# Kernel tuning notes

Measured on AMD Instinct MI355X. Metric: run time of the kernel, lower is better.

## Reference

```python
import jax, jax.numpy as jnp
import numpy as np
from jax import lax

NUM_HEADS = 8


def setup_inputs() -> dict:
    key = jax.random.key(0)
    ks = jax.random.split(key, 6)
    B, L, Hd = 4, 4096, 512
    S = 45  # factor * ceil(ln(L)) = 5 * 9
    x = jax.random.normal(ks[0], (B, L, Hd), dtype=jnp.float32)
    scale = 1.0 / np.sqrt(Hd)
    Wq = jax.random.normal(ks[1], (Hd, Hd), dtype=jnp.float32) * scale
    Wk = jax.random.normal(ks[2], (Hd, Hd), dtype=jnp.float32) * scale
    Wv = jax.random.normal(ks[3], (Hd, Hd), dtype=jnp.float32) * scale
    Wo = jax.random.normal(ks[4], (Hd, Hd), dtype=jnp.float32) * scale
    index_sample = jax.random.randint(ks[5], (L, S), 0, L, dtype=jnp.int32)
    return {"x": x, "Wq": Wq, "Wk": Wk, "Wv": Wv, "Wo": Wo,
            "index_sample": index_sample}


def reference(x, Wq, Wk, Wv, Wo, index_sample):
    B, L, Hd = x.shape
    H = NUM_HEADS
    D = Hd // H
    S = index_sample.shape[1]
    u = S  # n_top active queries = factor*ceil(ln(L))

    def split_heads(t):  # [B,L,Hd] -> [B,H,L,D]
        return t.reshape(B, L, H, D).transpose(0, 2, 1, 3)

    q = split_heads(x @ Wq)
    k = split_heads(x @ Wk)
    v = split_heads(x @ Wv)

    scale = 1.0 / jnp.sqrt(jnp.asarray(D, dtype=x.dtype))

    # sampled key gather: [B,H,L,S,D]
    K_samp = k[:, :, index_sample, :]
    # sampled scores per query: [B,H,L,S]
    QK_samp = jnp.einsum('bhld,bhlsd->bhls', q, K_samp)
    # sparsity measurement: max - mean over sampled keys
    M = QK_samp.max(axis=-1) - QK_samp.mean(axis=-1)  # [B,H,L]
    _, top_idx = lax.top_k(M, u)                      # [B,H,u]

    # full attention only for active queries
    Qr = jnp.take_along_axis(q, top_idx[..., None], axis=2)   # [B,H,u,D]
    scores = jnp.einsum('bhud,bhld->bhul', Qr, k) * scale     # [B,H,u,L]
    attn = jax.nn.softmax(scores, axis=-1)
    ctx_sel = jnp.einsum('bhul,bhld->bhud', attn, v)          # [B,H,u,D]

    # inactive queries get mean(V); scatter active results in
    context = jnp.broadcast_to(v.mean(axis=2, keepdims=True), (B, H, L, D))
    b_idx = jnp.arange(B)[:, None, None]
    h_idx = jnp.arange(H)[None, :, None]
    context = context.at[b_idx, h_idx, top_idx].set(ctx_sel)

    out = context.transpose(0, 2, 1, 3).reshape(B, L, Hd) @ Wo
    return out
```

## Files before the change

kernel.cpp:

```cpp
#include <hip/hip_runtime.h>
#include <cmath>

#define SS 45
#define FSPLIT 16

typedef __attribute__((ext_vector_type(8))) _Float16 half8;
typedef __attribute__((ext_vector_type(4))) float float4v;
typedef __attribute__((ext_vector_type(8))) unsigned short ushort8v;

__device__ inline unsigned short f16b(float f) {
    union { _Float16 h; unsigned short u; } c;
    c.h = (_Float16)f;
    return c.u;
}
__device__ inline float f16back(unsigned short u) {
    union { _Float16 h; unsigned short u; } c;
    c.u = u;
    return (float)c.h;
}

__device__ __forceinline__ void async16(const void* g, void* l) {
    __builtin_amdgcn_global_load_lds(
        (const __attribute__((address_space(1))) void*)g,
        (__attribute__((address_space(3))) void*)l, 16, 0, 0);
}

template <int CTRL>
__device__ __forceinline__ float dppadd(float v) {
    int x = __builtin_amdgcn_mov_dpp(__float_as_int(v), CTRL, 0xF, 0xF, true);
    return v + __int_as_float(x);
}
template <int CTRL>
__device__ __forceinline__ float dppmax(float v) {
    int x = __builtin_amdgcn_mov_dpp(__float_as_int(v), CTRL, 0xF, 0xF, true);
    return fmaxf(v, __int_as_float(x));
}

__device__ __forceinline__ unsigned int fmono(float f) {
    unsigned int u = __float_as_uint(f);
    return (u & 0x80000000u) ? ~u : (u | 0x80000000u);
}

__global__ __launch_bounds__(256) void convW_kernel(
    const float* __restrict__ Wq, const float* __restrict__ Wk, const float* __restrict__ Wv,
    unsigned short* __restrict__ WTh, unsigned short* __restrict__ WTl,
    float* __restrict__ vmp)
{
    int bid = blockIdx.x;
    if (bid < 768) {
        int zy = bid >> 8;
        int bxy = bid & 255;
        const float* W = (zy == 0) ? Wq : (zy == 1) ? Wk : Wv;
        unsigned short* th = WTh + (size_t)zy * 262144;
        unsigned short* tl = WTl + (size_t)zy * 262144;
        __shared__ float t[32][33];
        int bx = bxy & 15, by = bxy >> 4;
        int tx = threadIdx.x & 31, ty = threadIdx.x >> 5;
        for (int i = ty; i < 32; i += 8) t[i][tx] = W[(size_t)(by * 32 + i) * 512 + bx * 32 + tx];
        __syncthreads();
        for (int i = ty; i < 32; i += 8) {
            float f = t[tx][i];
            unsigned short h = f16b(f);
            unsigned short lo = f16b(f - f16back(h));
            th[(size_t)(bx * 32 + i) * 512 + by * 32 + tx] = h;
            tl[(size_t)(bx * 32 + i) * 512 + by * 32 + tx] = lo;
        }
    } else {
        for (int i = threadIdx.x; i < 2048; i += 256) vmp[i] = 0.f;
    }
}

__global__ __launch_bounds__(512, 2) void qkv8_kernel(
    const float* __restrict__ X,
    const unsigned short* __restrict__ WTh, const unsigned short* __restrict__ WTl,
    float* __restrict__ Q, float* __restrict__ K, float* __restrict__ V,
    float* __restrict__ vmp)
{
    __shared__ unsigned short lds[73728];

    int wave = threadIdx.x >> 6;
    int lane = threadIdx.x & 63;
    int m0blk = blockIdx.x * 256;
    int n0blk = blockIdx.y * 128;
    int fr = lane & 15;
    int C = lane >> 4;
    int srow = lane >> 2;
    int sslot = lane & 3;
    int mrb = (wave >> 1) * 64;
    int nrb = (wave & 1) * 64;

    const unsigned short* gbB[5];
    gbB[0] = WTh;
    gbB[1] = WTl;
    gbB[2] = WTh + 262144;
    gbB[3] = WTl + 262144;
    gbB[4] = WTh + 524288;

    int rloc0 = wave * 32 + srow;
    int rloc1 = wave * 32 + 16 + srow;
    int Cp0 = sslot ^ ((rloc0 >> 1) & 3);
    int Cp1 = sslot ^ ((rloc1 >> 1) & 3);
    const float* xr0 = X + (size_t)(m0blk + rloc0) * 512 + Cp0 * 8;
    const float* xr1 = X + (size_t)(m0blk + rloc1) * 512 + Cp1 * 8;

    float4v accq[4][4], acck[4][4], accv[4][4];
    #pragma unroll
    for (int i = 0; i < 4; i++)
        #pragma unroll
        for (int j = 0; j < 4; j++) {
            accq[i][j] = (float4v){0.f, 0.f, 0.f, 0.f};
            acck[i][j] = (float4v){0.f, 0.f, 0.f, 0.f};
            accv[i][j] = (float4v){0.f, 0.f, 0.f, 0.f};
        }

    auto stageB = [&](int buf, int k0) {
        int rloc = wave * 16 + srow;
        int Cp = sslot ^ ((rloc >> 1) & 3);
        #pragma unroll
        for (int t = 0; t < 5; t++) {
            const unsigned short* g = gbB[t] + (size_t)(n0blk + rloc) * 512 + k0 + Cp * 8;
            async16(g, lds + buf * 36864 + 16384 + t * 4096 + wave * 512);
        }
    };

    float4 xv[2][2];
    auto loadX = [&](int k0) {
        xv[0][0] = *(const float4*)(xr0 + k0);
        xv[0][1] = *(const float4*)(xr0 + k0 + 4);
        xv[1][0] = *(const float4*)(xr1 + k0);
        xv[1][1] = *(const float4*)(xr1 + k0 + 4);
    };
    auto writeA = [&](int buf) {
        #pragma unroll
        for (int inst = 0; inst < 2; inst++) {
            const float* f = (const float*)&xv[inst][0];
            ushort8v hv, lv;
            #pragma unroll
            for (int e = 0; e < 8; e++) {
                unsigned short h = f16b(f[e]);
                hv[e] = h;
                lv[e] = f16b(f[e] - f16back(h));
            }
            unsigned short* dsth = lds + buf * 36864 + (wave * 32 + inst * 16) * 32 + lane * 8;
            *(ushort8v*)dsth = hv;
            *(ushort8v*)(dsth + 8192) = lv;
        }
    };

    loadX(0);
    stageB(0, 0);
    writeA(0);
    asm volatile("s_waitcnt vmcnt(0)" ::: "memory");
    asm volatile("s_waitcnt lgkmcnt(0)" ::: "memory");
    __builtin_amdgcn_s_barrier();

    for (int kk = 0; kk < 16; kk++) {
        const unsigned short* Lb = lds + (kk & 1) * 36864;
        int nbuf = (kk + 1) & 1;
        int nk0 = (kk + 1) * 32;

        if (kk < 15) {
            loadX(nk0);
            stageB(nbuf, nk0);
        }

        half8 A_h[4], A_l[4];
        #pragma unroll
        for (int i = 0; i < 4; i++) {
            int R = mrb + i * 16 + fr;
            int sl = C ^ ((R >> 1) & 3);
            A_h[i] = *(const half8*)(Lb + R * 32 + sl * 8);
            A_l[i] = *(const half8*)(Lb + 8192 + R * 32 + sl * 8);
        }
        #pragma unroll
        for (int j = 0; j < 4; j++) {
            int R = nrb + j * 16 + fr;
            int sl = C ^ ((R >> 1) & 3);
            int off = R * 32 + sl * 8;
            half8 Bqh = *(const half8*)(Lb + 16384 + off);
            half8 Bql = *(const half8*)(Lb + 20480 + off);
            half8 Bkh = *(const half8*)(Lb + 24576 + off);
            half8 Bkl = *(const half8*)(Lb + 28672 + off);
            half8 Bvh = *(const half8*)(Lb + 32768 + off);
            #pragma unroll
            for (int i = 0; i < 4; i++) {
                accq[i][j] = __builtin_amdgcn_mfma_f32_16x16x32_f16(A_h[i], Bqh, accq[i][j], 0, 0, 0);
                accq[i][j] = __builtin_amdgcn_mfma_f32_16x16x32_f16(A_h[i], Bql, accq[i][j], 0, 0, 0);
                accq[i][j] = __builtin_amdgcn_mfma_f32_16x16x32_f16(A_l[i], Bqh, accq[i][j], 0, 0, 0);
                acck[i][j] = __builtin_amdgcn_mfma_f32_16x16x32_f16(A_h[i], Bkh, acck[i][j], 0, 0, 0);
                acck[i][j] = __builtin_amdgcn_mfma_f32_16x16x32_f16(A_h[i], Bkl, acck[i][j], 0, 0, 0);
                acck[i][j] = __builtin_amdgcn_mfma_f32_16x16x32_f16(A_l[i], Bkh, acck[i][j], 0, 0, 0);
                accv[i][j] = __builtin_amdgcn_mfma_f32_16x16x32_f16(A_h[i], Bvh, accv[i][j], 0, 0, 0);
            }
        }

        if (kk < 15) {
            writeA(nbuf);
            asm volatile("s_waitcnt vmcnt(0)" ::: "memory");
            asm volatile("s_waitcnt lgkmcnt(0)" ::: "memory");
            __builtin_amdgcn_s_barrier();
        }
    }

    int hh = n0blk + nrb;
    int hd = hh >> 6;
    int bb0 = (m0blk + mrb) >> 12;
    {
        float cs[4];
        #pragma unroll
        for (int j = 0; j < 4; j++) {
            float s = 0.f;
            #pragma unroll
            for (int i = 0; i < 4; i++)
                #pragma unroll
                for (int r = 0; r < 4; r++) s += accv[i][j][r];
            s += __shfl_xor(s, 16, 64);
            s += __shfl_xor(s, 32, 64);
            cs[j] = s;
        }
        if (C == 0) {
            #pragma unroll
            for (int j = 0; j < 4; j++)
                atomicAdd(vmp + ((size_t)(bb0 * 8 + hd) * 64) + j * 16 + fr, cs[j]);
        }
    }

    int rbase = C * 4;
    int m0 = m0blk + mrb;
    #pragma unroll
    for (int i = 0; i < 4; i++)
        #pragma unroll
        for (int r = 0; r < 4; r++) {
            int rg = m0 + i * 16 + rbase + r;
            int bb = rg >> 12, l = rg & 4095;
            size_t rowoff = ((size_t)(bb * 8 + hd) * 4096 + l) * 64;
            #pragma unroll
            for (int j = 0; j < 4; j++) Q[rowoff + j * 16 + fr] = accq[i][j][r];
            #pragma unroll
            for (int j = 0; j < 4; j++) K[rowoff + j * 16 + fr] = acck[i][j][r];
            #pragma unroll
            for (int j = 0; j < 4; j++) V[rowoff + j * 16 + fr] = accv[i][j][r];
        }
}

__global__ __launch_bounds__(1024) void m_topk_kernel(
    const float* __restrict__ Q, const float* __restrict__ K,
    const int* __restrict__ idx, unsigned long long* __restrict__ cand)
{
    __shared__ unsigned long long keys[512];

    int bh = blockIdx.x & 31;
    int c = blockIdx.x >> 5;
    int wave = threadIdx.x >> 6;
    int lane = threadIdx.x & 63;
    int g = lane >> 3;
    int t = lane & 7;
    const float* kb = K + (size_t)bh * 4096 * 64;

    for (int ii = 0; ii < 32; ii++) {
        int l = c * 512 + wave * 32 + ii;
        int inst = bh * 4096 + l;
        float4 qa = *(const float4*)(Q + (size_t)inst * 64 + t * 4);
        float4 qb = *(const float4*)(Q + (size_t)inst * 64 + 32 + t * 4);
        const int* irow = idx + (size_t)l * SS;
        int jv[6];
        #pragma unroll
        for (int it = 0; it < 6; it++) {
            int s = it * 8 + g;
            jv[it] = irow[(it == 5 && g >= 5) ? 0 : s];
        }
        float4 kva[6], kvb[6];
        #pragma unroll
        for (int it = 0; it < 6; it++) {
            kva[it] = *(const float4*)(kb + (size_t)jv[it] * 64 + t * 4);
            kvb[it] = *(const float4*)(kb + (size_t)jv[it] * 64 + 32 + t * 4);
        }
        float maxv = -1e30f, sum = 0.f, p0 = 0.f;
        #pragma unroll
        for (int it = 0; it < 6; it++) {
            float p = qa.x * kva[it].x;
            p = fmaf(qa.y, kva[it].y, p);
            p = fmaf(qa.z, kva[it].z, p);
            p = fmaf(qa.w, kva[it].w, p);
            p = fmaf(qb.x, kvb[it].x, p);
            p = fmaf(qb.y, kvb[it].y, p);
            p = fmaf(qb.z, kvb[it].z, p);
            p = fmaf(qb.w, kvb[it].w, p);
            p = dppadd<0xB1>(p);
            p = dppadd<0x4E>(p);
            p = dppadd<0x141>(p);
            if (it == 0) p0 = p;
            maxv = fmaxf(maxv, p);
            sum += p;
        }
        maxv = dppmax<0x128>(maxv);
        maxv = fmaxf(maxv, __shfl_xor(maxv, 16, 64));
        maxv = fmaxf(maxv, __shfl_xor(maxv, 32, 64));
        sum = dppadd<0x128>(sum);
        sum += __shfl_xor(sum, 16, 64);
        sum += __shfl_xor(sum, 32, 64);
        float p0b = __shfl(p0, 0, 64);
        if (lane == 0) {
            float Mval = maxv - (sum - 3.f * p0b) * (1.f / 45.f);
            keys[wave * 32 + ii] =
                ((unsigned long long)fmono(Mval) << 32) | (unsigned int)(4095 - l);
        }
    }
    __syncthreads();

    int tid = threadIdx.x;
    for (int k = 2; k <= 512; k <<= 1)
        for (int j = k >> 1; j > 0; j >>= 1) {
            if (tid < 512) {
                int i0 = tid;
                int ixj = i0 ^ j;
                if (ixj > i0) {
                    unsigned long long a = keys[i0], b = keys[ixj];
                    bool asc = (i0 & k) != 0;
                    if (asc ? (a > b) : (a < b)) { keys[i0] = b; keys[ixj] = a; }
                }
            }
            __syncthreads();
        }
    if (tid < SS) cand[((size_t)bh * 8 + c) * SS + tid] = keys[tid];
}

__global__ __launch_bounds__(256) void topk_merge_base_kernel(
    const unsigned long long* __restrict__ cand, int* __restrict__ tidx,
    const float* __restrict__ vmp, const float* __restrict__ Wo,
    float* __restrict__ vmean, float* __restrict__ base)
{
    int bid = blockIdx.x;
    int tid = threadIdx.x;
    if (bid < 32) {
        __shared__ unsigned long long keys[512];
        for (int i = tid; i < 512; i += 256) {
            unsigned long long v = 0ull;
            if (i < 8 * SS) {
                int cc = i / SS, r = i - cc * SS;
                v = cand[((size_t)bid * 8 + cc) * SS + r];
            }
            keys[i] = v;
        }
        __syncthreads();
        for (int k = 2; k <= 512; k <<= 1)
            for (int j = k >> 1; j > 0; j >>= 1) {
                for (int i0 = tid; i0 < 512; i0 += 256) {
                    int ixj = i0 ^ j;
                    if (ixj > i0) {
                        unsigned long long a = keys[i0], b = keys[ixj];
                        bool asc = (i0 & k) != 0;
                        if (asc ? (a > b) : (a < b)) { keys[i0] = b; keys[ixj] = a; }
                    }
                }
                __syncthreads();
            }
        if (tid < SS) tidx[bid * SS + tid] = 4095 - (int)(keys[tid] & 0xFFFFFFFFu);
    } else {
        int b = bid - 32;
        __shared__ float vmS[512];
        for (int i = tid; i < 512; i += 256) {
            float s = vmp[(size_t)b * 512 + i] * (1.f / 4096.f);
            vmS[i] = s;
            vmean[(size_t)b * 512 + i] = s;
        }
        __syncthreads();
        for (int jj = tid; jj < 512; jj += 256) {
            float s = 0.f;
            for (int i = 0; i < 512; i++) s += vmS[i] * Wo[(size_t)i * 512 + jj];
            base[(size_t)b * 512 + jj] = s;
        }
    }
}

__global__ __launch_bounds__(256) void attn_fill_kernel(
    const float* __restrict__ Q, const float* __restrict__ K, const float* __restrict__ V,
    const int* __restrict__ tidx,
    float* __restrict__ Opart, float* __restrict__ mpart, float* __restrict__ lpart,
    const float4* __restrict__ base4, float4* __restrict__ out4)
{
    int bid = blockIdx.x;
    if (bid >= 512) {
        int i0 = (bid - 512) * 1024 + threadIdx.x;
        #pragma unroll
        for (int k = 0; k < 4; k++) {
            int i = i0 + k * 256;
            int b = i >> 19;
            int j4 = i & 127;
            out4[i] = base4[b * 128 + j4];
        }
        return;
    }
    int split = bid & 15;
    int bh = bid >> 4;
    int L0 = split * (4096 / FSPLIT);

    __shared__ float Qs[48][68];
    __shared__ float Ks[64][68];
    __shared__ float Vs[64][68];
    __shared__ float Ps[48][68];
    __shared__ int tS[48];

    int tid = threadIdx.x;
    int lane = tid & 63, w = tid >> 6;
    if (tid < 48) tS[tid] = (tid < SS) ? tidx[bh * SS + tid] : 0;
    __syncthreads();
    for (int u = w; u < 48; u += 4)
        Qs[u][lane] = Q[((size_t)bh * 4096 + tS[u]) * 64 + lane];

    int ug = tid >> 4, lg = tid & 15;
    float mrun[3], lrun[3], O[3][4];
    #pragma unroll
    for (int i = 0; i < 3; i++) {
        mrun[i] = -1e30f; lrun[i] = 0.f;
        #pragma unroll
        for (int j = 0; j < 4; j++) O[i][j] = 0.f;
    }

    for (int tt = 0; tt < 4096 / FSPLIT / 64; tt++) {
        int lbase = L0 + tt * 64;
        if (tt > 0) __syncthreads();
        for (int r = w; r < 64; r += 4) {
            Ks[r][lane] = K[((size_t)bh * 4096 + lbase + r) * 64 + lane];
            Vs[r][lane] = V[((size_t)bh * 4096 + lbase + r) * 64 + lane];
        }
        __syncthreads();

        {
            float acc[3][4];
            #pragma unroll
            for (int i = 0; i < 3; i++)
                #pragma unroll
                for (int j = 0; j < 4; j++) acc[i][j] = 0.f;
            for (int d0 = 0; d0 < 64; d0 += 4) {
                float4 a[3], b[4];
                #pragma unroll
                for (int i = 0; i < 3; i++) a[i] = *(float4*)&Qs[ug * 3 + i][d0];
                #pragma unroll
                for (int j = 0; j < 4; j++) b[j] = *(float4*)&Ks[lg * 4 + j][d0];
                #pragma unroll
                for (int i = 0; i < 3; i++)
                    #pragma unroll
                    for (int j = 0; j < 4; j++)
                        acc[i][j] += a[i].x * b[j].x + a[i].y * b[j].y + a[i].z * b[j].z + a[i].w * b[j].w;
            }
            #pragma unroll
            for (int i = 0; i < 3; i++) {
                #pragma unroll
                for (int j = 0; j < 4; j++) acc[i][j] *= 0.125f;
                float tm = fmaxf(fmaxf(acc[i][0], acc[i][1]), fmaxf(acc[i][2], acc[i][3]));
                tm = fmaxf(tm, __shfl_xor(tm, 1, 64));
                tm = fmaxf(tm, __shfl_xor(tm, 2, 64));
                tm = fmaxf(tm, __shfl_xor(tm, 4, 64));
                tm = fmaxf(tm, __shfl_xor(tm, 8, 64));
                float nm = fmaxf(mrun[i], tm);
                float corr = __expf(mrun[i] - nm);
                float rs = 0.f;
                #pragma unroll
                for (int j = 0; j < 4; j++) {
                    float p = __expf(acc[i][j] - nm);
                    Ps[ug * 3 + i][lg * 4 + j] = p;
                    rs += p;
                }
                rs += __shfl_xor(rs, 1, 64);
                rs += __shfl_xor(rs, 2, 64);
                rs += __shfl_xor(rs, 4, 64);
                rs += __shfl_xor(rs, 8, 64);
                lrun[i] = lrun[i] * corr + rs;
                mrun[i] = nm;
                #pragma unroll
                for (int j = 0; j < 4; j++) O[i][j] *= corr;
            }
        }
        __syncthreads();

        {
            for (int l0 = 0; l0 < 64; l0 += 4) {
                float4 vr[4];
                #pragma unroll
                for (int r = 0; r < 4; r++) vr[r] = *(float4*)&Vs[l0 + r][lg * 4];
                #pragma unroll
                for (int i = 0; i < 3; i++) {
                    float4 pv = *(float4*)&Ps[ug * 3 + i][l0];
                    #pragma unroll
                    for (int j = 0; j < 4; j++) {
                        float vj0 = (&vr[0].x)[j], vj1 = (&vr[1].x)[j];
                        float vj2 = (&vr[2].x)[j], vj3 = (&vr[3].x)[j];
                        O[i][j] = fmaf(pv.x, vj0, fmaf(pv.y, vj1, fmaf(pv.z, vj2, fmaf(pv.w, vj3, O[i][j]))));
                    }
                }
            }
        }
    }

    {
        #pragma unroll
        for (int i = 0; i < 3; i++) {
            int u = ug * 3 + i;
            if (u < SS) {
                size_t pbase = ((size_t)(bh * FSPLIT + split) * SS + u);
                if (lg == 0) { mpart[pbase] = mrun[i]; lpart[pbase] = lrun[i]; }
                #pragma unroll
                for (int j = 0; j < 4; j++)
                    Opart[pbase * 64 + lg * 4 + j] = O[i][j];
            }
        }
    }
}

__global__ __launch_bounds__(256) void combine_kernel(
    const float* __restrict__ Opart, const float* __restrict__ mpart, const float* __restrict__ lpart,
    const float* __restrict__ vmean, const float* __restrict__ Wo,
    const int* __restrict__ tidx, float* __restrict__ out)
{
    int rr = blockIdx.x;
    int bh = rr / SS, u = rr % SS;
    int h = bh & 7, b = bh >> 3;
    __shared__ float dS[64];
    int tid = threadIdx.x;
    if (tid < 64) {
        float m = -1e30f;
        #pragma unroll
        for (int s = 0; s < FSPLIT; s++)
            m = fmaxf(m, mpart[(size_t)(bh * FSPLIT + s) * SS + u]);
        float den = 0.f, num = 0.f;
        #pragma unroll
        for (int s = 0; s < FSPLIT; s++) {
            size_t pbase = (size_t)(bh * FSPLIT + s) * SS + u;
            float wgt = __expf(mpart[pbase] - m);
            den += wgt * lpart[pbase];
            num += wgt * Opart[pbase * 64 + tid];
        }
        dS[tid] = num / den - vmean[(size_t)bh * 64 + tid];
    }
    __syncthreads();
    int l = tidx[rr];
    float* orow = out + ((size_t)b * 4096 + l) * 512;
    for (int j = tid; j < 512; j += 256) {
        float s = 0.f;
        #pragma unroll
        for (int dd = 0; dd < 64; dd++) s += dS[dd] * Wo[(size_t)(h * 64 + dd) * 512 + j];
        atomicAdd(orow + j, s);
    }
}

extern "C" void kernel_launch(void* const* d_in, const int* in_sizes, int n_in,
                              void* d_out, int out_size, void* d_ws, size_t ws_size,
                              hipStream_t stream)
{
    const float* x  = (const float*)d_in[0];
    const float* Wq = (const float*)d_in[1];
    const float* Wk = (const float*)d_in[2];
    const float* Wv = (const float*)d_in[3];
    const float* Wo = (const float*)d_in[4];
    const int*  idx = (const int*)d_in[5];
    float* out = (float*)d_out;

    float* W = (float*)d_ws;
    float* Q = W;
    float* K = W + 8388608;
    float* V = W + 16777216;
    unsigned short* WTh = (unsigned short*)(W + 33554432);
    unsigned short* WTl = (unsigned short*)(W + 33947648);
    float* vmp = W + 34340864;

    float* Opart = W + 25296896;
    float* mpart = W + 26771456;
    float* lpart = W + 26794496;
    float* vmean = W + 33439744;
    float* base  = W + 33441792;
    int*   tidx  = (int*)(W + 33443840);
    unsigned long long* cand = (unsigned long long*)(W + 33445280);

    convW_kernel<<<769, 256, 0, stream>>>(Wq, Wk, Wv, WTh, WTl, vmp);
    qkv8_kernel<<<dim3(64, 4), 512, 0, stream>>>(x, WTh, WTl, Q, K, V, vmp);
    m_topk_kernel<<<256, 1024, 0, stream>>>(Q, K, idx, cand);
    topk_merge_base_kernel<<<36, 256, 0, stream>>>(cand, tidx, vmp, Wo, vmean, base);
    attn_fill_kernel<<<512 + 2048, 256, 0, stream>>>(Q, K, V, tidx, Opart, mpart, lpart,
                                                     (const float4*)base, (float4*)out);
    combine_kernel<<<1440, 256, 0, stream>>>(Opart, mpart, lpart, vmean, Wo, tidx, out);
}
```

Before: 386.1 us.

## Reshuffle kernel stages and fuse split combine into attention via last-block counter

New measurement: 972.8 us. 152% more time.

```diff
diff --git a/kernel.cpp b/kernel.cpp
--- a/kernel.cpp
+++ b/kernel.cpp
@@ -44,7 +44,7 @@
 __global__ __launch_bounds__(256) void convW_kernel(
     const float* __restrict__ Wq, const float* __restrict__ Wk, const float* __restrict__ Wv,
     unsigned short* __restrict__ WTh, unsigned short* __restrict__ WTl,
-    float* __restrict__ vmp)
+    float* __restrict__ vmp, int* __restrict__ cnt)
 {
     int bid = blockIdx.x;
     if (bid < 768) {
@@ -67,6 +67,7 @@
         }
     } else {
         for (int i = threadIdx.x; i < 2048; i += 256) vmp[i] = 0.f;
+        if (threadIdx.x < 32) cnt[threadIdx.x] = 0;
     }
 }
 
@@ -243,11 +244,31 @@
         }
 }
 
-__global__ __launch_bounds__(1024) void m_topk_kernel(
+__global__ __launch_bounds__(1024) void m_topk_base_kernel(
     const float* __restrict__ Q, const float* __restrict__ K,
-    const int* __restrict__ idx, unsigned long long* __restrict__ cand)
+    const int* __restrict__ idx, unsigned long long* __restrict__ cand,
+    const float* __restrict__ vmp, const float* __restrict__ Wo,
+    float* __restrict__ vmean, float* __restrict__ base)
 {
     __shared__ unsigned long long keys[512];
+    __shared__ float vmS[512];
+
+    int tid = threadIdx.x;
+    if (blockIdx.x >= 256) {
+        int b = blockIdx.x - 256;
+        for (int i = tid; i < 512; i += 1024) {
+            float s = vmp[(size_t)b * 512 + i] * (1.f / 4096.f);
+            vmS[i] = s;
+            vmean[(size_t)b * 512 + i] = s;
+        }
+        __syncthreads();
+        for (int jj = tid; jj < 512; jj += 1024) {
+            float s = 0.f;
+            for (int i = 0; i < 512; i++) s += vmS[i] * Wo[(size_t)i * 512 + jj];
+            base[(size_t)b * 512 + jj] = s;
+        }
+        return;
+    }
 
     int bh = blockIdx.x & 31;
     int c = blockIdx.x >> 5;
@@ -308,7 +329,6 @@
     }
     __syncthreads();
 
-    int tid = threadIdx.x;
     for (int k = 2; k <= 512; k <<= 1)
         for (int j = k >> 1; j > 0; j >>= 1) {
             if (tid < 512) {
@@ -325,63 +345,14 @@
     if (tid < SS) cand[((size_t)bh * 8 + c) * SS + tid] = keys[tid];
 }
 
-__global__ __launch_bounds__(256) void topk_merge_base_kernel(
+__global__ __launch_bounds__(256) void topk_merge_fill_kernel(
     const unsigned long long* __restrict__ cand, int* __restrict__ tidx,
-    const float* __restrict__ vmp, const float* __restrict__ Wo,
-    float* __restrict__ vmean, float* __restrict__ base)
+    const float4* __restrict__ base4, float4* __restrict__ out4)
 {
     int bid = blockIdx.x;
     int tid = threadIdx.x;
-    if (bid < 32) {
-        __shared__ unsigned long long keys[512];
-        for (int i = tid; i < 512; i += 256) {
-            unsigned long long v = 0ull;
-            if (i < 8 * SS) {
-                int cc = i / SS, r = i - cc * SS;
-                v = cand[((size_t)bid * 8 + cc) * SS + r];
-            }
-            keys[i] = v;
-        }
-        __syncthreads();
-        for (int k = 2; k <= 512; k <<= 1)
-            for (int j = k >> 1; j > 0; j >>= 1) {
-                for (int i0 = tid; i0 < 512; i0 += 256) {
-                    int ixj = i0 ^ j;
-                    if (ixj > i0) {
-                        unsigned long long a = keys[i0], b = keys[ixj];
-                        bool asc = (i0 & k) != 0;
-                        if (asc ? (a > b) : (a < b)) { keys[i0] = b; keys[ixj] = a; }
-                    }
-                }
-                __syncthreads();
-            }
-        if (tid < SS) tidx[bid * SS + tid] = 4095 - (int)(keys[tid] & 0xFFFFFFFFu);
-    } else {
-        int b = bid - 32;
-        __shared__ float vmS[512];
-        for (int i = tid; i < 512; i += 256) {
-            float s = vmp[(size_t)b * 512 + i] * (1.f / 4096.f);
-            vmS[i] = s;
-            vmean[(size_t)b * 512 + i] = s;
-        }
-        __syncthreads();
-        for (int jj = tid; jj < 512; jj += 256) {
-            float s = 0.f;
-            for (int i = 0; i < 512; i++) s += vmS[i] * Wo[(size_t)i * 512 + jj];
-            base[(size_t)b * 512 + jj] = s;
-        }
-    }
-}
-
-__global__ __launch_bounds__(256) void attn_fill_kernel(
-    const float* __restrict__ Q, const float* __restrict__ K, const float* __restrict__ V,
-    const int* __restrict__ tidx,
-    float* __restrict__ Opart, float* __restrict__ mpart, float* __restrict__ lpart,
-    const float4* __restrict__ base4, float4* __restrict__ out4)
-{
-    int bid = blockIdx.x;
-    if (bid >= 512) {
-        int i0 = (bid - 512) * 1024 + threadIdx.x;
+    if (bid >= 32) {
+        int i0 = (bid - 32) * 1024 + tid;
         #pragma unroll
         for (int k = 0; k < 4; k++) {
             int i = i0 + k * 256;
@@ -391,6 +362,39 @@
         }
         return;
     }
+    __shared__ unsigned long long keys[512];
+    for (int i = tid; i < 512; i += 256) {
+        unsigned long long v = 0ull;
+        if (i < 8 * SS) {
+            int cc = i / SS, r = i - cc * SS;
+            v = cand[((size_t)bid * 8 + cc) * SS + r];
+        }
+        keys[i] = v;
+    }
+    __syncthreads();
+    for (int k = 2; k <= 512; k <<= 1)
+        for (int j = k >> 1; j > 0; j >>= 1) {
+            for (int i0 = tid; i0 < 512; i0 += 256) {
+                int ixj = i0 ^ j;
+                if (ixj > i0) {
+                    unsigned long long a = keys[i0], b = keys[ixj];
+                    bool asc = (i0 & k) != 0;
+                    if (asc ? (a > b) : (a < b)) { keys[i0] = b; keys[ixj] = a; }
+                }
+            }
+            __syncthreads();
+        }
+    if (tid < SS) tidx[bid * SS + tid] = 4095 - (int)(keys[tid] & 0xFFFFFFFFu);
+}
+
+__global__ __launch_bounds__(256) void attn_combine_kernel(
+    const float* __restrict__ Q, const float* __restrict__ K, const float* __restrict__ V,
+    const int* __restrict__ tidx,
+    float* __restrict__ Opart, float* __restrict__ mpart, float* __restrict__ lpart,
+    const float* __restrict__ vmean, const float* __restrict__ Wo,
+    int* __restrict__ cnt, float* __restrict__ out)
+{
+    int bid = blockIdx.x;
     int split = bid & 15;
     int bh = bid >> 4;
     int L0 = split * (4096 / FSPLIT);
@@ -400,6 +404,8 @@
     __shared__ float Vs[64][68];
     __shared__ float Ps[48][68];
     __shared__ int tS[48];
+    __shared__ float dS[64];
+    __shared__ int amLast;
 
     int tid = threadIdx.x;
     int lane = tid & 63, w = tid >> 6;
@@ -506,41 +512,41 @@
             }
         }
     }
-}
-
-__global__ __launch_bounds__(256) void combine_kernel(
-    const float* __restrict__ Opart, const float* __restrict__ mpart, const float* __restrict__ lpart,
-    const float* __restrict__ vmean, const float* __restrict__ Wo,
-    const int* __restrict__ tidx, float* __restrict__ out)
-{
-    int rr = blockIdx.x;
-    int bh = rr / SS, u = rr % SS;
+
+    __threadfence();
+    __syncthreads();
+    if (tid == 0) amLast = (atomicAdd(&cnt[bh], 1) == FSPLIT - 1);
+    __syncthreads();
+    if (!amLast) return;
+    __threadfence();
+
     int h = bh & 7, b = bh >> 3;
-    __shared__ float dS[64];
-    int tid = threadIdx.x;
-    if (tid < 64) {
-        float m = -1e30f;
-        #pragma unroll
-        for (int s = 0; s < FSPLIT; s++)
-            m = fmaxf(m, mpart[(size_t)(bh * FSPLIT + s) * SS + u]);
-        float den = 0.f, num = 0.f;
-        #pragma unroll
-        for (int s = 0; s < FSPLIT; s++) {
-            size_t pbase = (size_t)(bh * FSPLIT + s) * SS + u;
-            float wgt = __expf(mpart[pbase] - m);
-            den += wgt * lpart[pbase];
-            num += wgt * Opart[pbase * 64 + tid];
-        }
-        dS[tid] = num / den - vmean[(size_t)bh * 64 + tid];
-    }
-    __syncthreads();
-    int l = tidx[rr];
-    float* orow = out + ((size_t)b * 4096 + l) * 512;
-    for (int j = tid; j < 512; j += 256) {
-        float s = 0.f;
-        #pragma unroll
-        for (int dd = 0; dd < 64; dd++) s += dS[dd] * Wo[(size_t)(h * 64 + dd) * 512 + j];
-        atomicAdd(orow + j, s);
+    for (int u = 0; u < SS; u++) {
+        if (tid < 64) {
+            float m = -1e30f;
+            #pragma unroll
+            for (int s = 0; s < FSPLIT; s++)
+                m = fmaxf(m, mpart[(size_t)(bh * FSPLIT + s) * SS + u]);
+            float den = 0.f, num = 0.f;
+            #pragma unroll
+            for (int s = 0; s < FSPLIT; s++) {
+                size_t pbase = (size_t)(bh * FSPLIT + s) * SS + u;
+                float wgt = __expf(mpart[pbase] - m);
+                den += wgt * lpart[pbase];
+                num += wgt * Opart[pbase * 64 + tid];
+            }
+            dS[tid] = num / den - vmean[(size_t)bh * 64 + tid];
+        }
+        __syncthreads();
+        int l = tidx[bh * SS + u];
+        float* orow = out + ((size_t)b * 4096 + l) * 512;
+        for (int j = tid; j < 512; j += 256) {
+            float s = 0.f;
+            #pragma unroll
+            for (int dd = 0; dd < 64; dd++) s += dS[dd] * Wo[(size_t)(h * 64 + dd) * 512 + j];
+            atomicAdd(orow + j, s);
+        }
+        __syncthreads();
     }
 }
 
@@ -571,12 +577,12 @@
     float* base  = W + 33441792;
     int*   tidx  = (int*)(W + 33443840);
     unsigned long long* cand = (unsigned long long*)(W + 33445280);
-
-    convW_kernel<<<769, 256, 0, stream>>>(Wq, Wk, Wv, WTh, WTl, vmp);
+    int*   cnt   = (int*)(W + 33468320);
+
+    convW_kernel<<<769, 256, 0, stream>>>(Wq, Wk, Wv, WTh, WTl, vmp, cnt);
     qkv8_kernel<<<dim3(64, 4), 512, 0, stream>>>(x, WTh, WTl, Q, K, V, vmp);
-    m_topk_kernel<<<256, 1024, 0, stream>>>(Q, K, idx, cand);
-    topk_merge_base_kernel<<<36, 256, 0, stream>>>(cand, tidx, vmp, Wo, vmean, base);
-    attn_fill_kernel<<<512 + 2048, 256, 0, stream>>>(Q, K, V, tidx, Opart, mpart, lpart,
-                                                     (const float4*)base, (float4*)out);
-    combine_kernel<<<1440, 256, 0, stream>>>(Opart, mpart, lpart, vmean, Wo, tidx, out);
-}
+    m_topk_base_kernel<<<260, 1024, 0, stream>>>(Q, K, idx, cand, vmp, Wo, vmean, base);
+    topk_merge_fill_kernel<<<32 + 2048, 256, 0, stream>>>(cand, tidx, (const float4*)base, (float4*)out);
+    attn_combine_kernel<<<512, 256, 0, stream>>>(Q, K, V, tidx, Opart, mpart, lpart,
+                                                 vmean, Wo, cnt, out);
+}
```
